# Kernel optimization log

Measured on AMD Instinct MI355X. Metric: run time of the kernel, lower is better.

Reference implementation:

```python
import jax, jax.numpy as jnp
import numpy as np
import math

B, T, C, N = 2, 2048, 1024, 16  # batch, seq, h_dim, n_heads
D = C // N

def setup_inputs() -> dict:
    key = jax.random.key(0)
    k1, k2, k3 = jax.random.split(key, 3)
    x = jax.random.normal(k1, (B, T, C), dtype=jnp.float32)
    Wqkv = jax.random.normal(k2, (C, 3 * C), dtype=jnp.float32) * (1.0 / math.sqrt(C))
    bqkv = jnp.zeros((3 * C,), dtype=jnp.float32)
    Wproj = jax.random.normal(k3, (C, C), dtype=jnp.float32) * (1.0 / math.sqrt(C))
    bproj = jnp.zeros((C,), dtype=jnp.float32)
    return {"x": x, "Wqkv": Wqkv, "bqkv": bqkv, "Wproj": Wproj, "bproj": bproj}

def reference(x, Wqkv, bqkv, Wproj, bproj):
    B_, T_, C_ = x.shape
    N_, D_ = N, C_ // N
    qkv = x @ Wqkv + bqkv                                  # (B,T,3C)
    q, k, v = jnp.split(qkv, 3, axis=-1)
    q = q.reshape(B_, T_, N_, D_).transpose(0, 2, 1, 3)    # (B,N,T,D)
    k = k.reshape(B_, T_, N_, D_).transpose(0, 2, 1, 3)
    v = v.reshape(B_, T_, N_, D_).transpose(0, 2, 1, 3)
    # causal mask: lower-triangular ones, broadcast over (B, 1, T, T)
    mask = jnp.tril(jnp.ones((T_, T_), dtype=jnp.float32))[None, None]
    weights = jnp.einsum('bntd,bnsd->bnts', q, k) / math.sqrt(D_)
    # faithful to original: adds tiny 1e-9 to masked entries (NOT -inf)
    weights = weights + (1.0 - mask) * 1e-9
    normalized = jax.nn.softmax(weights, axis=-1)
    attn = jnp.einsum('bnts,bnsd->bntd', normalized, v)    # (B,N,T,D)
    attn = attn.transpose(0, 2, 1, 3).reshape(B_, T_, N_ * D_)
    out = attn @ Wproj + bproj                              # (B,T,C)
    return out
```

## Files before the change

### kernel.cpp

```cpp
#include <hip/hip_runtime.h>
#include <hip/hip_bf16.h>

#define BB 2
#define TT 2048
#define CC 1024
#define NHEAD 16
#define DHEAD 64
#define MM (BB*TT)
#define KVB 128

using bf16 = __hip_bfloat16;
typedef __bf16 bf16x8 __attribute__((ext_vector_type(8)));
typedef __bf16 bf16x4 __attribute__((ext_vector_type(4)));
typedef float f32x4 __attribute__((ext_vector_type(4)));

static __device__ __forceinline__ bf16 f2b(float f) { return __float2bfloat16(f); }
static __device__ __forceinline__ float fast_exp2(float f) { return __builtin_amdgcn_exp2f(f); }

static __device__ __forceinline__ void gload16(const bf16* g, bf16* l) {
  __builtin_amdgcn_global_load_lds((__attribute__((address_space(1))) const void*)g,
                                   (__attribute__((address_space(3))) void*)l, 16, 0, 0);
}

__global__ __launch_bounds__(256)
void k_prep(const float* __restrict__ x, bf16* __restrict__ Xb,
            const float* __restrict__ Wqkv, bf16* __restrict__ WqkvT,
            const float* __restrict__ Wproj, bf16* __restrict__ WprojT)
{
  int bid = blockIdx.x;
  const int tid = threadIdx.x;
  if (bid < 1024) {
    int base = bid * 1024 + tid;
#pragma unroll
    for (int k = 0; k < 4; ++k) {
      int i = base + k * 256;
      float4 v = reinterpret_cast<const float4*>(x)[i];
      bf16 o[4] = { f2b(v.x), f2b(v.y), f2b(v.z), f2b(v.w) };
      reinterpret_cast<uint2*>(Xb)[i] = *reinterpret_cast<uint2*>(o);
    }
    return;
  }
  bid -= 1024;
  __shared__ float tile[32][33];
  const float* W; bf16* WT; int R, Cc, bx, by;
  if (bid < 3072) {
    W = Wqkv;  WT = WqkvT;  R = CC; Cc = 3*CC;
    bx = bid % 96; by = bid / 96;
  } else {
    bid -= 3072;
    W = Wproj; WT = WprojT; R = CC; Cc = CC;
    bx = bid % 32; by = bid / 32;
  }
  int c0 = bx * 32, r0 = by * 32;
  int tx = tid & 31, ty = tid >> 5;
#pragma unroll
  for (int i = 0; i < 4; ++i)
    tile[ty + 8*i][tx] = W[(size_t)(r0 + ty + 8*i) * Cc + c0 + tx];
  __syncthreads();
#pragma unroll
  for (int i = 0; i < 4; ++i)
    WT[(size_t)(c0 + ty + 8*i) * R + r0 + tx] = f2b(tile[tx][ty + 8*i]);
}

#define NTK 32
__global__ __launch_bounds__(512, 2)
void k_gemm_qkv(const bf16* __restrict__ Ag, const bf16* __restrict__ Bg,
                const float* __restrict__ bias,
                bf16* __restrict__ Qb, bf16* __restrict__ Kb, bf16* __restrict__ Vb)
{
  const int tid = threadIdx.x;
  const int w = tid >> 6, l = tid & 63;
  const int l16 = l & 15, l4 = l >> 4;
  const int wr = w >> 2, wc = w & 3;

  const int flat = blockIdx.x;
  const int xcd = flat & 7, local = flat >> 3;
  const int bx = (xcd & 1) * 6 + local % 6;
  const int by = (xcd >> 1) * 8 + local / 6;
  const int m0 = by * 128, n0 = bx * 256;

  __shared__ __align__(16) bf16 sm[36864];

  f32x4 acc[4][4];
#pragma unroll
  for (int m = 0; m < 4; ++m)
#pragma unroll
    for (int n = 0; n < 4; ++n) acc[m][n] = 0.f;

  const int srow = tid >> 2;
  const int scol = ((tid & 3) ^ ((tid >> 3) & 3)) * 8;

#define STAGE(buf, kt) do {                                                            \
    const int kb = (kt) * 32 + scol;                                                   \
    gload16(&Ag[(size_t)(m0 +       srow) * CC + kb], &sm[(buf)*12288        + w*512]);\
    gload16(&Bg[(size_t)(n0 +       srow) * CC + kb], &sm[(buf)*12288 + 4096 + w*512]);\
    gload16(&Bg[(size_t)(n0 + 128 + srow) * CC + kb], &sm[(buf)*12288 + 8192 + w*512]);\
  } while (0)

  STAGE(0, 0);
  STAGE(1, 1);
  STAGE(2, 2);
  asm volatile("s_waitcnt vmcnt(6)" ::: "memory");
  __builtin_amdgcn_s_barrier();

  const int slotA = (l4 ^ ((l16 >> 1) & 3)) * 8;
  const int aoff = wr * 2048 + l16 * 32 + slotA;
  const int boff = 4096 + wc * 2048 + l16 * 32 + slotA;

  int rb = 0;
  for (int kt = 0; kt < NTK; ++kt) {
    const int base = rb * 12288;

    bf16x8 af[4], bfr[4];
#pragma unroll
    for (int m = 0; m < 4; ++m)
      af[m] = *reinterpret_cast<const bf16x8*>(&sm[base + aoff + m*512]);
#pragma unroll
    for (int n = 0; n < 4; ++n)
      bfr[n] = *reinterpret_cast<const bf16x8*>(&sm[base + boff + n*512]);
    __builtin_amdgcn_s_setprio(1);
#pragma unroll
    for (int m = 0; m < 4; ++m)
#pragma unroll
      for (int n = 0; n < 4; ++n)
        acc[m][n] = __builtin_amdgcn_mfma_f32_16x16x32_bf16(af[m], bfr[n], acc[m][n], 0, 0, 0);
    __builtin_amdgcn_s_setprio(0);

    __builtin_amdgcn_s_barrier();
    if (kt + 3 < NTK) {
      STAGE(rb, kt + 3);
      asm volatile("s_waitcnt vmcnt(6)" ::: "memory");
    } else if (kt + 2 < NTK) {
      asm volatile("s_waitcnt vmcnt(3)" ::: "memory");
    } else if (kt + 1 < NTK) {
      asm volatile("s_waitcnt vmcnt(0)" ::: "memory");
    }
    __builtin_amdgcn_s_barrier();
    rb = (rb + 1 == 3) ? 0 : rb + 1;
  }
#undef STAGE

  const int ccol = n0 + wc * 64;
  const int which = ccol >> 10;
  if (which == 2) {
#pragma unroll
    for (int m = 0; m < 4; ++m)
#pragma unroll
      for (int n = 0; n < 4; ++n) {
        int gc = ccol + n*16 + l16;
        float bv = bias[gc];
        int c = gc & (CC-1), head = c >> 6, d = c & 63;
        int t0r = m0 + wr*64 + m*16 + l4*4;
        int b = t0r >> 11, t = t0r & (TT-1);
        bf16x4 pk;
#pragma unroll
        for (int j = 0; j < 4; ++j) pk[j] = (__bf16)(acc[m][n][j] + bv);
        *reinterpret_cast<bf16x4*>(
            &Vb[(((size_t)b*NHEAD + head)*DHEAD + d)*TT + t]) = pk;
      }
  } else {
    bf16* __restrict__ dst = (which == 0) ? Qb : Kb;
    const float qsc = (which == 0) ? 0.125f * 1.4426950408889634f : 1.0f;
#pragma unroll
    for (int m = 0; m < 4; ++m)
#pragma unroll
      for (int n = 0; n < 4; ++n) {
        int gc = ccol + n*16 + l16;
        float bv = bias[gc];
        int c = gc & (CC-1), head = c >> 6, d = c & 63;
#pragma unroll
        for (int j = 0; j < 4; ++j) {
          int gr = m0 + wr*64 + m*16 + l4*4 + j;
          int b = gr >> 11, t = gr & (TT-1);
          dst[(((size_t)b*NHEAD + head)*TT + t)*DHEAD + d] = f2b((acc[m][n][j] + bv) * qsc);
        }
      }
  }
}

__global__ __launch_bounds__(512, 1)
void k_gemm_proj(const bf16* __restrict__ Ag, const bf16* __restrict__ Bg,
                 const float* __restrict__ bias, float* __restrict__ outF)
{
  const int tid = threadIdx.x;
  const int w = tid >> 6, l = tid & 63;
  const int l16 = l & 15, l4 = l >> 4;
  const int wr = w >> 2, wc = w & 3;

  const int flat = blockIdx.x;
  const int swz = (flat & 7) * 32 + (flat >> 3);
  const int bx = swz >> 5, by = swz & 31;
  const int m0 = by * 128, n0 = bx * 128;

  __shared__ __align__(16) bf16 sm[24576];

  f32x4 acc[4][2];
#pragma unroll
  for (int m = 0; m < 4; ++m)
#pragma unroll
    for (int n = 0; n < 2; ++n) acc[m][n] = 0.f;

  const int srow = tid >> 2;
  const int scol = ((tid & 3) ^ ((tid >> 3) & 3)) * 8;

#define STAGE(buf, kt) do {                                                            \
    const int kb = (kt) * 32 + scol;                                                   \
    gload16(&Ag[(size_t)(m0 + srow) * CC + kb], &sm[(buf)*8192        + w*512]);       \
    gload16(&Bg[(size_t)(n0 + srow) * CC + kb], &sm[(buf)*8192 + 4096 + w*512]);       \
  } while (0)

  STAGE(0, 0);
  STAGE(1, 1);
  STAGE(2, 2);
  asm volatile("s_waitcnt vmcnt(4)" ::: "memory");
  __builtin_amdgcn_s_barrier();

  const int slotA = (l4 ^ ((l16 >> 1) & 3)) * 8;
  const int aoff = wr * 2048 + l16 * 32 + slotA;
  const int boff = 4096 + wc * 1024 + l16 * 32 + slotA;

  int rb = 0;
  for (int kt = 0; kt < NTK; ++kt) {
    const int base = rb * 8192;

    bf16x8 af[4], bfr[2];
#pragma unroll
    for (int m = 0; m < 4; ++m)
      af[m] = *reinterpret_cast<const bf16x8*>(&sm[base + aoff + m*512]);
#pragma unroll
    for (int n = 0; n < 2; ++n)
      bfr[n] = *reinterpret_cast<const bf16x8*>(&sm[base + boff + n*512]);
    __builtin_amdgcn_s_setprio(1);
#pragma unroll
    for (int m = 0; m < 4; ++m)
#pragma unroll
      for (int n = 0; n < 2; ++n)
        acc[m][n] = __builtin_amdgcn_mfma_f32_16x16x32_bf16(af[m], bfr[n], acc[m][n], 0, 0, 0);
    __builtin_amdgcn_s_setprio(0);

    __builtin_amdgcn_s_barrier();
    if (kt + 3 < NTK) {
      STAGE(rb, kt + 3);
      asm volatile("s_waitcnt vmcnt(4)" ::: "memory");
    } else if (kt + 2 < NTK) {
      asm volatile("s_waitcnt vmcnt(2)" ::: "memory");
    } else if (kt + 1 < NTK) {
      asm volatile("s_waitcnt vmcnt(0)" ::: "memory");
    }
    __builtin_amdgcn_s_barrier();
    rb = (rb + 1 == 3) ? 0 : rb + 1;
  }
#undef STAGE

#pragma unroll
  for (int m = 0; m < 4; ++m)
#pragma unroll
    for (int n = 0; n < 2; ++n) {
      int gc = n0 + wc*32 + n*16 + l16;
      float bv = bias[gc];
#pragma unroll
      for (int j = 0; j < 4; ++j) {
        int gr = m0 + wr*64 + m*16 + l4*4 + j;
        outF[(size_t)gr * CC + gc] = acc[m][n][j] + bv;
      }
    }
}

__global__ __launch_bounds__(512, 2)
void k_attn(const bf16* __restrict__ Qg, const bf16* __restrict__ Kg,
            const bf16* __restrict__ VTg, bf16* __restrict__ Aout)
{
  const int tid  = threadIdx.x;
  const int wave = tid >> 6, lane = tid & 63;
  const int l16 = lane & 15, l4 = lane >> 4;

  const int flat = blockIdx.x;
  const int xcd = flat & 7, i6 = flat >> 3;
  const int bn = xcd*4 + (i6 >> 4);
  const int q0 = (i6 & 15) * 128;
  const int b = bn >> 4, h = bn & (NHEAD-1);

  __shared__ __align__(16) bf16 KsF[128*64];
  __shared__ __align__(16) bf16 VtF[64*128];
  __shared__ __align__(16) bf16 PlF[8*16*128];

  const size_t hb = (size_t)bn * TT * DHEAD;
  const bf16* __restrict__ Kbase = Kg + hb;
  const bf16* __restrict__ Vbase = VTg + hb;

  bf16x8 qf[2];
#pragma unroll
  for (int kk = 0; kk < 2; ++kk)
    qf[kk] = *reinterpret_cast<const bf16x8*>(
        &Qg[hb + (size_t)(q0 + wave*16 + l16) * DHEAD + kk*32 + l4*8]);

  f32x4 o[4];
#pragma unroll
  for (int n = 0; n < 4; ++n) o[n] = 0.f;
  float mrun = -1e30f, lrun = 0.f;

  const int krow = tid >> 2, kq = tid & 3;
  const int vrow = tid >> 3, vq = tid & 7;

  bf16x8 kreg[2], vreg[2];
#pragma unroll
  for (int i = 0; i < 2; ++i) {
    kreg[i] = *reinterpret_cast<const bf16x8*>(&Kbase[(size_t)krow * DHEAD + kq*16 + 8*i]);
    vreg[i] = *reinterpret_cast<const bf16x8*>(&Vbase[(size_t)vrow * TT + vq*16 + 8*i]);
  }
#pragma unroll
  for (int i = 0; i < 2; ++i) {
    *reinterpret_cast<bf16x8*>(&KsF[krow*64 + ((kq*2 + i) ^ (krow & 7))*8]) = kreg[i];
    *reinterpret_cast<bf16x8*>(&VtF[vrow*128 + ((vq*2 + i) ^ (vrow & 7))*8]) = vreg[i];
  }

  bf16* PlW = &PlF[wave * 2048];

  for (int t0 = 0; t0 < TT; t0 += KVB) {
    __syncthreads();
    const bool more = (t0 + KVB < TT);
    if (more) {
#pragma unroll
      for (int i = 0; i < 2; ++i) {
        kreg[i] = *reinterpret_cast<const bf16x8*>(
            &Kbase[(size_t)(t0 + KVB + krow) * DHEAD + kq*16 + 8*i]);
        vreg[i] = *reinterpret_cast<const bf16x8*>(
            &Vbase[(size_t)vrow * TT + t0 + KVB + vq*16 + 8*i]);
      }
    }

    f32x4 s[8];
#pragma unroll
    for (int n = 0; n < 8; ++n) s[n] = 0.f;
    __builtin_amdgcn_s_setprio(1);
#pragma unroll
    for (int n = 0; n < 8; ++n) {
      bf16x8 kf0 = *reinterpret_cast<const bf16x8*>(
          &KsF[(n*16 + l16)*64 + ((l4    ) ^ (l16 & 7))*8]);
      bf16x8 kf1 = *reinterpret_cast<const bf16x8*>(
          &KsF[(n*16 + l16)*64 + ((4 + l4) ^ (l16 & 7))*8]);
      s[n] = __builtin_amdgcn_mfma_f32_16x16x32_bf16(kf0, qf[0], s[n], 0, 0, 0);
      s[n] = __builtin_amdgcn_mfma_f32_16x16x32_bf16(kf1, qf[1], s[n], 0, 0, 0);
    }
    __builtin_amdgcn_s_setprio(0);

    float mx[8];
#pragma unroll
    for (int n = 0; n < 8; ++n)
      mx[n] = fmaxf(fmaxf(s[n][0], s[n][1]), fmaxf(s[n][2], s[n][3]));
    float m01 = fmaxf(mx[0], mx[1]), m23 = fmaxf(mx[2], mx[3]);
    float m45 = fmaxf(mx[4], mx[5]), m67 = fmaxf(mx[6], mx[7]);
    float pm = fmaxf(fmaxf(m01, m23), fmaxf(m45, m67));
    pm = fmaxf(pm, __shfl_xor(pm, 16, 64));
    pm = fmaxf(pm, __shfl_xor(pm, 32, 64));

    if (!__all(pm <= mrun + 8.f)) {
      float mn = fmaxf(mrun, pm);
      float corr = fast_exp2(mrun - mn);
      mrun = mn;
      lrun *= corr;
      float cj[4];
#pragma unroll
      for (int j = 0; j < 4; ++j)
        cj[j] = __shfl(corr, ((lane >> 4) << 2) + j, 64);
#pragma unroll
      for (int n = 0; n < 4; ++n)
#pragma unroll
        for (int j = 0; j < 4; ++j) o[n][j] *= cj[j];
    }

    float ps[4] = {0.f, 0.f, 0.f, 0.f};
#pragma unroll
    for (int n = 0; n < 8; ++n) {
      bf16x4 pk;
#pragma unroll
      for (int j = 0; j < 4; ++j) {
        float pv = fast_exp2(s[n][j] - mrun);
        ps[j] += pv;
        pk[j] = (__bf16)pv;
      }
      *reinterpret_cast<bf16x4*>(
          &PlW[l16*128 + ((2*n + (l4 >> 1)) ^ (l16 & 7))*8 + (l4 & 1)*4]) = pk;
    }
    float psum = (ps[0] + ps[1]) + (ps[2] + ps[3]);
    psum += __shfl_xor(psum, 16, 64);
    psum += __shfl_xor(psum, 32, 64);
    lrun += psum;

    bf16x8 pf[4];
#pragma unroll
    for (int kk = 0; kk < 4; ++kk)
      pf[kk] = *reinterpret_cast<const bf16x8*>(
          &PlW[l16*128 + ((4*kk + l4) ^ (l16 & 7))*8]);
    __builtin_amdgcn_s_setprio(1);
#pragma unroll
    for (int n = 0; n < 4; ++n)
#pragma unroll
      for (int kk = 0; kk < 4; ++kk) {
        bf16x8 vf = *reinterpret_cast<const bf16x8*>(
            &VtF[(n*16 + l16)*128 + ((4*kk + l4) ^ (l16 & 7))*8]);
        o[n] = __builtin_amdgcn_mfma_f32_16x16x32_bf16(pf[kk], vf, o[n], 0, 0, 0);
      }
    __builtin_amdgcn_s_setprio(0);

    __syncthreads();
    if (more) {
#pragma unroll
      for (int i = 0; i < 2; ++i) {
        *reinterpret_cast<bf16x8*>(&KsF[krow*64 + ((kq*2 + i) ^ (krow & 7))*8]) = kreg[i];
        *reinterpret_cast<bf16x8*>(&VtF[vrow*128 + ((vq*2 + i) ^ (vrow & 7))*8]) = vreg[i];
      }
    }
  }

  float linv = 1.0f / lrun;
  float lj[4];
#pragma unroll
  for (int j = 0; j < 4; ++j)
    lj[j] = __shfl(linv, ((lane >> 4) << 2) + j, 64);
#pragma unroll
  for (int j = 0; j < 4; ++j) {
    int gt = q0 + wave*16 + l4*4 + j;
#pragma unroll
    for (int n = 0; n < 4; ++n)
      Aout[((size_t)(b*TT + gt))*CC + h*DHEAD + n*16 + l16] = f2b(o[n][j] * lj[j]);
  }
}

extern "C" void kernel_launch(void* const* d_in, const int* in_sizes, int n_in,
                              void* d_out, int out_size, void* d_ws, size_t ws_size,
                              hipStream_t stream)
{
  const float* x     = (const float*)d_in[0];
  const float* Wqkv  = (const float*)d_in[1];
  const float* bqkv  = (const float*)d_in[2];
  const float* Wproj = (const float*)d_in[3];
  const float* bproj = (const float*)d_in[4];
  float* out = (float*)d_out;

  char* p = (char*)d_ws;
  bf16* Xb     = (bf16*)p;  p += (size_t)MM*CC*2;
  bf16* WqkvT  = (bf16*)p;  p += (size_t)3*CC*CC*2;
  bf16* WprojT = (bf16*)p;  p += (size_t)CC*CC*2;
  bf16* Qb     = (bf16*)p;  p += (size_t)MM*CC*2;
  bf16* Kb     = (bf16*)p;  p += (size_t)MM*CC*2;
  bf16* Vb     = (bf16*)p;  p += (size_t)MM*CC*2;
  bf16* Attn   = (bf16*)p;  p += (size_t)MM*CC*2;

  k_prep<<<5120, 256, 0, stream>>>(x, Xb, Wqkv, WqkvT, Wproj, WprojT);
  k_gemm_qkv<<<384, 512, 0, stream>>>(Xb, WqkvT, bqkv, Qb, Kb, Vb);
  k_attn<<<512, 512, 0, stream>>>(Qb, Kb, Vb, Attn);
  k_gemm_proj<<<256, 512, 0, stream>>>(Attn, WprojT, bproj, out);
}
```

Measured before the change: 120.1 us.

## Double-buffer K/V tiles with direct global-to-LDS loads in attention kernel

Replaces register-staged K/V prefetch with asynchronous global_load_lds writes into a second LDS buffer, keeping the same XOR swizzle by permuting the global source addresses. This removes one barrier per iteration and the VGPR round trip for the staging. The P scratch buffer is halved by splitting the PV product into two 64-column halves interleaved with the exp computation. LDS use per block rises to about 80KB, which makes two blocks per CU tight, and correctness depends on vmcnt waits being emitted before the barrier.

```diff
diff --git a/kernel.cpp b/kernel.cpp
--- a/kernel.cpp
+++ b/kernel.cpp
@@ -280,9 +280,9 @@
   const int q0 = (i6 & 15) * 128;
   const int b = bn >> 4, h = bn & (NHEAD-1);
 
-  __shared__ __align__(16) bf16 KsF[128*64];
-  __shared__ __align__(16) bf16 VtF[64*128];
-  __shared__ __align__(16) bf16 PlF[8*16*128];
+  __shared__ __align__(16) bf16 KsF[2*128*64];
+  __shared__ __align__(16) bf16 VtF[2*64*128];
+  __shared__ __align__(16) bf16 PlF[8*16*64];
 
   const size_t hb = (size_t)bn * TT * DHEAD;
   const bf16* __restrict__ Kbase = Kg + hb;
@@ -299,35 +299,33 @@
   for (int n = 0; n < 4; ++n) o[n] = 0.f;
   float mrun = -1e30f, lrun = 0.f;
 
-  const int krow = tid >> 2, kq = tid & 3;
-  const int vrow = tid >> 3, vq = tid & 7;
-
-  bf16x8 kreg[2], vreg[2];
-#pragma unroll
-  for (int i = 0; i < 2; ++i) {
-    kreg[i] = *reinterpret_cast<const bf16x8*>(&Kbase[(size_t)krow * DHEAD + kq*16 + 8*i]);
-    vreg[i] = *reinterpret_cast<const bf16x8*>(&Vbase[(size_t)vrow * TT + vq*16 + 8*i]);
-  }
-#pragma unroll
-  for (int i = 0; i < 2; ++i) {
-    *reinterpret_cast<bf16x8*>(&KsF[krow*64 + ((kq*2 + i) ^ (krow & 7))*8]) = kreg[i];
-    *reinterpret_cast<bf16x8*>(&VtF[vrow*128 + ((vq*2 + i) ^ (vrow & 7))*8]) = vreg[i];
-  }
-
-  bf16* PlW = &PlF[wave * 2048];
+  const int krow0 = tid >> 3, kslot = tid & 7;
+  const int vrow0 = tid >> 4, vslot = tid & 15;
+
+#define ASTAGE(buf, tn) do {                                                              \
+    {                                                                                     \
+      int r0_ = krow0,      s0_ = (kslot ^ (r0_ & 7)) * 8;                                \
+      int r1_ = 64 + krow0, s1_ = (kslot ^ (r1_ & 7)) * 8;                                \
+      gload16(&Kbase[(size_t)((tn) + r0_) * DHEAD + s0_], &KsF[(buf)*8192        + wave*512]); \
+      gload16(&Kbase[(size_t)((tn) + r1_) * DHEAD + s1_], &KsF[(buf)*8192 + 4096 + wave*512]); \
+      int vr0_ = vrow0,      vs0_ = (vslot ^ (vr0_ & 7)) * 8;                             \
+      int vr1_ = 32 + vrow0, vs1_ = (vslot ^ (vr1_ & 7)) * 8;                             \
+      gload16(&Vbase[(size_t)vr0_ * TT + (tn) + vs0_], &VtF[(buf)*8192        + wave*512]);    \
+      gload16(&Vbase[(size_t)vr1_ * TT + (tn) + vs1_], &VtF[(buf)*8192 + 4096 + wave*512]);    \
+    }                                                                                     \
+  } while (0)
+
+  ASTAGE(0, 0);
+  __syncthreads();
+
+  bf16* PlW = &PlF[wave * 1024];
 
   for (int t0 = 0; t0 < TT; t0 += KVB) {
-    __syncthreads();
+    const int cur = (t0 >> 7) & 1;
     const bool more = (t0 + KVB < TT);
-    if (more) {
-#pragma unroll
-      for (int i = 0; i < 2; ++i) {
-        kreg[i] = *reinterpret_cast<const bf16x8*>(
-            &Kbase[(size_t)(t0 + KVB + krow) * DHEAD + kq*16 + 8*i]);
-        vreg[i] = *reinterpret_cast<const bf16x8*>(
-            &Vbase[(size_t)vrow * TT + t0 + KVB + vq*16 + 8*i]);
-      }
-    }
+    if (more) ASTAGE(cur ^ 1, t0 + KVB);
+
+    const int kbase = cur * 8192, vbase = cur * 8192;
 
     f32x4 s[8];
 #pragma unroll
@@ -336,9 +334,9 @@
 #pragma unroll
     for (int n = 0; n < 8; ++n) {
       bf16x8 kf0 = *reinterpret_cast<const bf16x8*>(
-          &KsF[(n*16 + l16)*64 + ((l4    ) ^ (l16 & 7))*8]);
+          &KsF[kbase + (n*16 + l16)*64 + ((l4    ) ^ (l16 & 7))*8]);
       bf16x8 kf1 = *reinterpret_cast<const bf16x8*>(
-          &KsF[(n*16 + l16)*64 + ((4 + l4) ^ (l16 & 7))*8]);
+          &KsF[kbase + (n*16 + l16)*64 + ((4 + l4) ^ (l16 & 7))*8]);
       s[n] = __builtin_amdgcn_mfma_f32_16x16x32_bf16(kf0, qf[0], s[n], 0, 0, 0);
       s[n] = __builtin_amdgcn_mfma_f32_16x16x32_bf16(kf1, qf[1], s[n], 0, 0, 0);
     }
@@ -371,47 +369,45 @@
 
     float ps[4] = {0.f, 0.f, 0.f, 0.f};
 #pragma unroll
-    for (int n = 0; n < 8; ++n) {
-      bf16x4 pk;
-#pragma unroll
-      for (int j = 0; j < 4; ++j) {
-        float pv = fast_exp2(s[n][j] - mrun);
-        ps[j] += pv;
-        pk[j] = (__bf16)pv;
+    for (int hh = 0; hh < 2; ++hh) {
+#pragma unroll
+      for (int n4 = 0; n4 < 4; ++n4) {
+        const int n = hh*4 + n4;
+        bf16x4 pk;
+#pragma unroll
+        for (int j = 0; j < 4; ++j) {
+          float pv = fast_exp2(s[n][j] - mrun);
+          ps[j] += pv;
+          pk[j] = (__bf16)pv;
+        }
+        *reinterpret_cast<bf16x4*>(
+            &PlW[l16*64 + ((2*n4 + (l4 >> 1)) ^ (l16 & 7))*8 + (l4 & 1)*4]) = pk;
       }
-      *reinterpret_cast<bf16x4*>(
-          &PlW[l16*128 + ((2*n + (l4 >> 1)) ^ (l16 & 7))*8 + (l4 & 1)*4]) = pk;
+      bf16x8 pf[2];
+#pragma unroll
+      for (int kkl = 0; kkl < 2; ++kkl)
+        pf[kkl] = *reinterpret_cast<const bf16x8*>(
+            &PlW[l16*64 + ((4*kkl + l4) ^ (l16 & 7))*8]);
+      __builtin_amdgcn_s_setprio(1);
+#pragma unroll
+      for (int n = 0; n < 4; ++n)
+#pragma unroll
+        for (int kkl = 0; kkl < 2; ++kkl) {
+          const int kk = hh*2 + kkl;
+          bf16x8 vf = *reinterpret_cast<const bf16x8*>(
+              &VtF[vbase + (n*16 + l16)*128 + ((4*kk + l4) ^ (l16 & 7))*8]);
+          o[n] = __builtin_amdgcn_mfma_f32_16x16x32_bf16(pf[kkl], vf, o[n], 0, 0, 0);
+        }
+      __builtin_amdgcn_s_setprio(0);
     }
     float psum = (ps[0] + ps[1]) + (ps[2] + ps[3]);
     psum += __shfl_xor(psum, 16, 64);
     psum += __shfl_xor(psum, 32, 64);
     lrun += psum;
 
-    bf16x8 pf[4];
-#pragma unroll
-    for (int kk = 0; kk < 4; ++kk)
-      pf[kk] = *reinterpret_cast<const bf16x8*>(
-          &PlW[l16*128 + ((4*kk + l4) ^ (l16 & 7))*8]);
-    __builtin_amdgcn_s_setprio(1);
-#pragma unroll
-    for (int n = 0; n < 4; ++n)
-#pragma unroll
-      for (int kk = 0; kk < 4; ++kk) {
-        bf16x8 vf = *reinterpret_cast<const bf16x8*>(
-            &VtF[(n*16 + l16)*128 + ((4*kk + l4) ^ (l16 & 7))*8]);
-        o[n] = __builtin_amdgcn_mfma_f32_16x16x32_bf16(pf[kk], vf, o[n], 0, 0, 0);
-      }
-    __builtin_amdgcn_s_setprio(0);
-
     __syncthreads();
-    if (more) {
-#pragma unroll
-      for (int i = 0; i < 2; ++i) {
-        *reinterpret_cast<bf16x8*>(&KsF[krow*64 + ((kq*2 + i) ^ (krow & 7))*8]) = kreg[i];
-        *reinterpret_cast<bf16x8*>(&VtF[vrow*128 + ((vq*2 + i) ^ (vrow & 7))*8]) = vreg[i];
-      }
-    }
-  }
+  }
+#undef ASTAGE
 
   float linv = 1.0f / lrun;
   float lj[4];
```

Result: no change. 118.1 us (-1.6%).
